# Optimization experiments

Hardware: AMD Instinct MI355X
Metric: run time of the kernel (lower is better)

Reference implementation:

```python
import jax, jax.numpy as jnp
import numpy as np

B, S, E, H = 2, 2048, 1024, 16
DH = E // H


def setup_inputs() -> dict:
    key = jax.random.key(0)
    ks = jax.random.split(key, 7)
    sc = 1.0 / np.sqrt(E)
    return {
        "x": jax.random.normal(ks[0], (B, S, E), dtype=jnp.float32),
        "Wq": jax.random.uniform(ks[1], (E, E), jnp.float32, -sc, sc),
        "bq": jax.random.uniform(ks[2], (E,), jnp.float32, -sc, sc),
        "Wk": jax.random.uniform(ks[3], (E, E), jnp.float32, -sc, sc),
        "bk": jax.random.uniform(ks[4], (E,), jnp.float32, -sc, sc),
        "Wv": jax.random.uniform(ks[5], (E, E), jnp.float32, -sc, sc),
        "bv": jax.random.uniform(ks[6], (E,), jnp.float32, -sc, sc),
    }


def reference(x, Wq, bq, Wk, bk, Wv, bv):
    b, s, _ = x.shape
    # torch Linear: y = x @ W.T + b
    q = (x @ Wq.T + bq).reshape(b, s, H, DH).transpose(0, 2, 1, 3)  # [B,H,S,Dh]
    k = (x @ Wk.T + bk).reshape(b, s, H, DH).transpose(0, 2, 1, 3)
    v = (x @ Wv.T + bv).reshape(b, s, H, DH).transpose(0, 2, 1, 3)
    # original einsum labels treat axis1 as 's' and axis2 as 'h'/'v':
    # scores: [B, S_q, H, S_k]  (softmax over keys, last axis)
    scores = jnp.einsum('bshd,bsvd->bhsv', q, k) / np.sqrt(DH)
    probs = jax.nn.softmax(scores, axis=-1)
    # out: [B, H, S, Dh] per original label permutation
    out = jnp.einsum('bhsv,bsvd->bshd', probs, v)
    # original reshapes WITHOUT transposing heads back (faithful quirk)
    return out.reshape(b, s, E)
```

## Files before the change

### kernel.cpp

```cpp
#include <hip/hip_runtime.h>
#include <hip/hip_bf16.h>

#define Bb 2
#define Ss 2048
#define Ee 1024
#define Hh 16
#define Dh 64
#define QSCALE 0.18033688011112042f

using u16 = unsigned short;
typedef __attribute__((ext_vector_type(8))) short short8;
typedef __attribute__((ext_vector_type(8))) u16 ushort8;
typedef __attribute__((ext_vector_type(4))) float f32x4;

#define GAS __attribute__((address_space(1)))
#define LAS __attribute__((address_space(3)))

__device__ __forceinline__ void gload16(const u16* g, u16* l) {
  __builtin_amdgcn_global_load_lds((const GAS unsigned int*)g,
                                   (LAS unsigned int*)l, 16, 0, 0);
}

__device__ __forceinline__ u16 f2bf(float f) {
  union { float f; unsigned u; } v;
  v.f = f;
  unsigned u = v.u;
  unsigned r = (u + 0x7FFFu + ((u >> 16) & 1u)) >> 16;
  return (u16)r;
}

__global__ __launch_bounds__(256) void cvt_all(
    const float* __restrict__ x, const float* __restrict__ wq,
    const float* __restrict__ wk, const float* __restrict__ wv,
    u16* __restrict__ xo, u16* __restrict__ wqo, u16* __restrict__ wko,
    u16* __restrict__ wvo) {
  const int b = blockIdx.x;
  const float* s;
  u16* d;
  int i;
  if (b < 2048) {
    s = x; d = xo; i = b * 256 + threadIdx.x;
  } else {
    const int wb = b - 2048;
    const int which = wb >> 9;
    s = which == 0 ? wq : (which == 1 ? wk : wv);
    d = which == 0 ? wqo : (which == 1 ? wko : wvo);
    i = (wb & 511) * 256 + threadIdx.x;
  }
  const float* p = s + (size_t)i * 8;
  ushort8 o;
#pragma unroll
  for (int j = 0; j < 8; ++j) o[j] = f2bf(p[j]);
  *(ushort8*)(d + (size_t)i * 8) = o;
}

__global__ __launch_bounds__(256) void qkv_gemm(
    const u16* __restrict__ Xb, const u16* __restrict__ Wcat,
    const float* __restrict__ bq, const float* __restrict__ bk,
    const float* __restrict__ bv,
    u16* __restrict__ Qo, u16* __restrict__ Ko, u16* __restrict__ Vo) {
  __shared__ u16 Ast[128][64];
  __shared__ u16 Bst[128][64];
  const int tid = threadIdx.x;
  const int lane = tid & 63;
  const int w = tid >> 6;
  const int wm = w >> 1, wn = w & 1;
  const int c = lane & 15, g = lane >> 4;
  const int m0 = blockIdx.y * 128;
  const int n0 = blockIdx.x * 128;
  const bool swapv = n0 >= 2048;

  f32x4 acc[4][4] = {};

  for (int kt = 0; kt < 16; ++kt) {
    const int k0 = kt * 64;
    __syncthreads();
#pragma unroll
    for (int i = 0; i < 4; ++i) {
      const int elem = i * 2048 + tid * 8;
      const int row = elem >> 6, col = elem & 63;
      const int lbase = i * 2048 + w * 512;
      gload16(Xb + (size_t)(m0 + row) * 1024 + k0 + col, &Ast[0][0] + lbase);
      gload16(Wcat + (size_t)(n0 + row) * 1024 + k0 + col, &Bst[0][0] + lbase);
    }
    __syncthreads();

#pragma unroll
    for (int ks = 0; ks < 2; ++ks) {
      short8 af[4], bf[4];
#pragma unroll
      for (int mf = 0; mf < 4; ++mf)
        af[mf] = *(const short8*)&Ast[wm * 64 + mf * 16 + c][ks * 32 + g * 8];
#pragma unroll
      for (int nf = 0; nf < 4; ++nf)
        bf[nf] = *(const short8*)&Bst[wn * 64 + nf * 16 + c][ks * 32 + g * 8];
      if (!swapv) {
#pragma unroll
        for (int mf = 0; mf < 4; ++mf)
#pragma unroll
          for (int nf = 0; nf < 4; ++nf)
            acc[mf][nf] = __builtin_amdgcn_mfma_f32_16x16x32_bf16(
                af[mf], bf[nf], acc[mf][nf], 0, 0, 0);
      } else {
#pragma unroll
        for (int mf = 0; mf < 4; ++mf)
#pragma unroll
          for (int nf = 0; nf < 4; ++nf)
            acc[mf][nf] = __builtin_amdgcn_mfma_f32_16x16x32_bf16(
                bf[nf], af[mf], acc[mf][nf], 0, 0, 0);
      }
    }
  }

  if (!swapv) {
    const int which = n0 >> 10;
    u16* Oo = which == 0 ? Qo : Ko;
    const float* bias = which == 0 ? bq : bk;
    const float scl = which == 0 ? QSCALE : 1.0f;
#pragma unroll
    for (int nf = 0; nf < 4; ++nf) {
      const int n = (n0 & 1023) + wn * 64 + nf * 16 + c;
      const float bval = bias[n];
      const int hh = n >> 6, dd = n & 63;
#pragma unroll
      for (int mf = 0; mf < 4; ++mf) {
#pragma unroll
        for (int r = 0; r < 4; ++r) {
          const int m = m0 + wm * 64 + mf * 16 + g * 4 + r;
          const int bb = m >> 11, ss = m & 2047;
          Oo[(((size_t)bb * Hh + hh) * Ss + ss) * Dh + dd] =
              f2bf((acc[mf][nf][r] + bval) * scl);
        }
      }
    }
  } else {
#pragma unroll
    for (int nf = 0; nf < 4; ++nf) {
#pragma unroll
      for (int r = 0; r < 4; ++r) {
        const int n = (n0 - 2048) + wn * 64 + nf * 16 + g * 4 + r;
        const float bval = bv[n];
        const int hh = n >> 6, dd = n & 63;
#pragma unroll
        for (int mf = 0; mf < 4; ++mf) {
          const int m = m0 + wm * 64 + mf * 16 + c;
          const int bb = m >> 11, ss = m & 2047;
          Vo[(((size_t)bb * Hh + hh) * Dh + dd) * Ss + ss] =
              f2bf(acc[mf][nf][r] + bval);
        }
      }
    }
  }
}

__global__ __launch_bounds__(256) void attn(
    const u16* __restrict__ Q, const u16* __restrict__ K,
    const u16* __restrict__ VT, float* __restrict__ out) {
  __shared__ u16 Kst[64][72];
  __shared__ u16 Vt[64][72];
  __shared__ u16 Pst[4][16][72];
  const int tid = threadIdx.x;
  const int lane = tid & 63;
  const int w = tid >> 6;
  const int c = lane & 15, g = lane >> 4;
  const int bh = blockIdx.y;
  const int q0 = blockIdx.x * 64;
  const u16* Qb = Q + (size_t)bh * Ss * Dh;
  const u16* Kb = K + (size_t)bh * Ss * Dh;
  const u16* VTb = VT + (size_t)bh * Ss * Dh;
  const int srow = tid >> 3, sseg = tid & 7;

  short8 aq[2];
  {
#pragma unroll
    for (int it = 0; it < 2; ++it)
      *(ushort8*)&Kst[it * 32 + srow][sseg * 8] =
          *(const ushort8*)(Qb + (size_t)(q0 + it * 32 + srow) * Dh + sseg * 8);
    __syncthreads();
    aq[0] = *(const short8*)&Kst[w * 16 + c][g * 8];
    aq[1] = *(const short8*)&Kst[w * 16 + c][32 + g * 8];
  }

  short8 ones;
#pragma unroll
  for (int j = 0; j < 8; ++j) ones[j] = (short)0x3F80;

  ushort8 kreg[2], vreg[2];
#pragma unroll
  for (int it = 0; it < 2; ++it) {
    kreg[it] = *(const ushort8*)(Kb + (size_t)(it * 32 + srow) * Dh + sseg * 8);
    vreg[it] = *(const ushort8*)(VTb + (size_t)(it * 32 + srow) * Ss + sseg * 8);
  }

  f32x4 oacc[4] = {};
  f32x4 lacc = {};

  for (int kt = 0; kt < 32; ++kt) {
    __syncthreads();
#pragma unroll
    for (int it = 0; it < 2; ++it) {
      *(ushort8*)&Kst[it * 32 + srow][sseg * 8] = kreg[it];
      *(ushort8*)&Vt[it * 32 + srow][sseg * 8] = vreg[it];
    }
    __syncthreads();
    if (kt < 31) {
      const int k0n = (kt + 1) * 64;
#pragma unroll
      for (int it = 0; it < 2; ++it) {
        kreg[it] = *(const ushort8*)(Kb + (size_t)(k0n + it * 32 + srow) * Dh + sseg * 8);
        vreg[it] = *(const ushort8*)(VTb + (size_t)(it * 32 + srow) * Ss + k0n + sseg * 8);
      }
    }

    f32x4 sc[4] = {};
    __builtin_amdgcn_s_setprio(1);
#pragma unroll
    for (int ks = 0; ks < 2; ++ks) {
#pragma unroll
      for (int nt = 0; nt < 4; ++nt) {
        short8 bk_ = *(const short8*)&Kst[nt * 16 + c][ks * 32 + g * 8];
        sc[nt] = __builtin_amdgcn_mfma_f32_16x16x32_bf16(aq[ks], bk_, sc[nt], 0, 0, 0);
      }
    }
    __builtin_amdgcn_s_setprio(0);

#pragma unroll
    for (int nt = 0; nt < 4; ++nt)
#pragma unroll
      for (int r = 0; r < 4; ++r) {
        float p = __builtin_amdgcn_exp2f(sc[nt][r]);
        Pst[w][g * 4 + r][nt * 16 + c] =
            (u16)(__builtin_bit_cast(unsigned, p) >> 16);
      }
    asm volatile("s_waitcnt lgkmcnt(0)" ::: "memory");
    __builtin_amdgcn_sched_barrier(0);

    __builtin_amdgcn_s_setprio(1);
#pragma unroll
    for (int ks = 0; ks < 2; ++ks) {
      short8 pa = *(const short8*)&Pst[w][c][ks * 32 + g * 8];
      lacc = __builtin_amdgcn_mfma_f32_16x16x32_bf16(pa, ones, lacc, 0, 0, 0);
#pragma unroll
      for (int nt2 = 0; nt2 < 4; ++nt2) {
        short8 bv_ = *(const short8*)&Vt[nt2 * 16 + c][ks * 32 + g * 8];
        oacc[nt2] = __builtin_amdgcn_mfma_f32_16x16x32_bf16(pa, bv_, oacc[nt2], 0, 0, 0);
      }
    }
    __builtin_amdgcn_s_setprio(0);
  }

  const size_t obase = (size_t)bh * Ss * Dh;
#pragma unroll
  for (int r = 0; r < 4; ++r) {
    const float inv = 1.0f / lacc[r];
    const int q = q0 + w * 16 + g * 4 + r;
#pragma unroll
    for (int nt2 = 0; nt2 < 4; ++nt2)
      out[obase + (size_t)q * Dh + nt2 * 16 + c] = oacc[nt2][r] * inv;
  }
}

extern "C" void kernel_launch(void* const* d_in, const int* in_sizes, int n_in,
                              void* d_out, int out_size, void* d_ws, size_t ws_size,
                              hipStream_t stream) {
  const float* x = (const float*)d_in[0];
  const float* Wq = (const float*)d_in[1];
  const float* bq = (const float*)d_in[2];
  const float* Wk = (const float*)d_in[3];
  const float* bk = (const float*)d_in[4];
  const float* Wv = (const float*)d_in[5];
  const float* bv = (const float*)d_in[6];
  float* out = (float*)d_out;

  if (ws_size < (size_t)(38u << 20)) return;
  char* ws = (char*)d_ws;
  u16* Qb = (u16*)(ws + (size_t)(0u << 20));
  u16* Kb = (u16*)(ws + (size_t)(8u << 20));
  u16* Vb = (u16*)(ws + (size_t)(16u << 20));
  u16* Xb = (u16*)(ws + (size_t)(24u << 20));
  u16* Wqb = (u16*)(ws + (size_t)(32u << 20));
  u16* Wkb = (u16*)(ws + (size_t)(34u << 20));
  u16* Wvb = (u16*)(ws + (size_t)(36u << 20));

  cvt_all<<<3584, 256, 0, stream>>>(x, Wq, Wk, Wv, Xb, Wqb, Wkb, Wvb);
  qkv_gemm<<<dim3(24, 32), 256, 0, stream>>>(Xb, Wqb, bq, bk, bv, Qb, Kb, Vb);
  attn<<<dim3(32, 32), 256, 0, stream>>>(Qb, Kb, Vb, out);
}
```

Before: 120.5 us.

## Load K/V fragments directly from global and double query rows per block

```diff
diff --git a/kernel.cpp b/kernel.cpp
--- a/kernel.cpp
+++ b/kernel.cpp
@@ -153,97 +153,102 @@
   }
 }
 
-__global__ __launch_bounds__(256) void attn(
+__global__ __launch_bounds__(256, 2) void attn(
     const u16* __restrict__ Q, const u16* __restrict__ K,
     const u16* __restrict__ VT, float* __restrict__ out) {
-  __shared__ u16 Kst[64][72];
-  __shared__ u16 Vt[64][72];
-  __shared__ u16 Pst[4][16][72];
+  __shared__ u16 Pst[4][2][16][72];
   const int tid = threadIdx.x;
   const int lane = tid & 63;
   const int w = tid >> 6;
   const int c = lane & 15, g = lane >> 4;
   const int bh = blockIdx.y;
-  const int q0 = blockIdx.x * 64;
+  const int q0 = blockIdx.x * 128;
   const u16* Qb = Q + (size_t)bh * Ss * Dh;
   const u16* Kb = K + (size_t)bh * Ss * Dh;
   const u16* VTb = VT + (size_t)bh * Ss * Dh;
-  const int srow = tid >> 3, sseg = tid & 7;
-
-  short8 aq[2];
-  {
-#pragma unroll
-    for (int it = 0; it < 2; ++it)
-      *(ushort8*)&Kst[it * 32 + srow][sseg * 8] =
-          *(const ushort8*)(Qb + (size_t)(q0 + it * 32 + srow) * Dh + sseg * 8);
-    __syncthreads();
-    aq[0] = *(const short8*)&Kst[w * 16 + c][g * 8];
-    aq[1] = *(const short8*)&Kst[w * 16 + c][32 + g * 8];
-  }
+
+  short8 aq[2][2];
+#pragma unroll
+  for (int h = 0; h < 2; ++h)
+#pragma unroll
+    for (int ks = 0; ks < 2; ++ks)
+      aq[h][ks] = *(const short8*)(Qb + (size_t)(q0 + h * 64 + w * 16 + c) * Dh +
+                                   ks * 32 + g * 8);
 
   short8 ones;
 #pragma unroll
   for (int j = 0; j < 8; ++j) ones[j] = (short)0x3F80;
 
-  ushort8 kreg[2], vreg[2];
-#pragma unroll
-  for (int it = 0; it < 2; ++it) {
-    kreg[it] = *(const ushort8*)(Kb + (size_t)(it * 32 + srow) * Dh + sseg * 8);
-    vreg[it] = *(const ushort8*)(VTb + (size_t)(it * 32 + srow) * Ss + sseg * 8);
-  }
-
-  f32x4 oacc[4] = {};
-  f32x4 lacc = {};
+  short8 kf[2][4];
+#pragma unroll
+  for (int ks = 0; ks < 2; ++ks)
+#pragma unroll
+    for (int nt = 0; nt < 4; ++nt)
+      kf[ks][nt] = *(const short8*)(Kb + (size_t)(nt * 16 + c) * Dh +
+                                    ks * 32 + g * 8);
+
+  f32x4 oacc[2][4] = {};
+  f32x4 lacc[2] = {};
 
   for (int kt = 0; kt < 32; ++kt) {
-    __syncthreads();
-#pragma unroll
-    for (int it = 0; it < 2; ++it) {
-      *(ushort8*)&Kst[it * 32 + srow][sseg * 8] = kreg[it];
-      *(ushort8*)&Vt[it * 32 + srow][sseg * 8] = vreg[it];
-    }
-    __syncthreads();
+    const int k0 = kt * 64;
+
+    short8 vf[2][4];
+#pragma unroll
+    for (int ks = 0; ks < 2; ++ks)
+#pragma unroll
+      for (int nt = 0; nt < 4; ++nt)
+        vf[ks][nt] = *(const short8*)(VTb + (size_t)(nt * 16 + c) * Ss + k0 +
+                                      ks * 32 + g * 8);
+
+    f32x4 sc[2][4] = {};
+    __builtin_amdgcn_s_setprio(1);
+#pragma unroll
+    for (int ks = 0; ks < 2; ++ks)
+#pragma unroll
+      for (int nt = 0; nt < 4; ++nt) {
+        sc[0][nt] = __builtin_amdgcn_mfma_f32_16x16x32_bf16(aq[0][ks], kf[ks][nt],
+                                                            sc[0][nt], 0, 0, 0);
+        sc[1][nt] = __builtin_amdgcn_mfma_f32_16x16x32_bf16(aq[1][ks], kf[ks][nt],
+                                                            sc[1][nt], 0, 0, 0);
+      }
+    __builtin_amdgcn_s_setprio(0);
+
     if (kt < 31) {
-      const int k0n = (kt + 1) * 64;
-#pragma unroll
-      for (int it = 0; it < 2; ++it) {
-        kreg[it] = *(const ushort8*)(Kb + (size_t)(k0n + it * 32 + srow) * Dh + sseg * 8);
-        vreg[it] = *(const ushort8*)(VTb + (size_t)(it * 32 + srow) * Ss + k0n + sseg * 8);
-      }
-    }
-
-    f32x4 sc[4] = {};
-    __builtin_amdgcn_s_setprio(1);
-#pragma unroll
-    for (int ks = 0; ks < 2; ++ks) {
-#pragma unroll
-      for (int nt = 0; nt < 4; ++nt) {
-        short8 bk_ = *(const short8*)&Kst[nt * 16 + c][ks * 32 + g * 8];
-        sc[nt] = __builtin_amdgcn_mfma_f32_16x16x32_bf16(aq[ks], bk_, sc[nt], 0, 0, 0);
-      }
-    }
-    __builtin_amdgcn_s_setprio(0);
-
-#pragma unroll
-    for (int nt = 0; nt < 4; ++nt)
-#pragma unroll
-      for (int r = 0; r < 4; ++r) {
-        float p = __builtin_amdgcn_exp2f(sc[nt][r]);
-        Pst[w][g * 4 + r][nt * 16 + c] =
-            (u16)(__builtin_bit_cast(unsigned, p) >> 16);
-      }
+#pragma unroll
+      for (int ks = 0; ks < 2; ++ks)
+#pragma unroll
+        for (int nt = 0; nt < 4; ++nt)
+          kf[ks][nt] = *(const short8*)(Kb + (size_t)(k0 + 64 + nt * 16 + c) * Dh +
+                                        ks * 32 + g * 8);
+    }
+
+#pragma unroll
+    for (int h = 0; h < 2; ++h)
+#pragma unroll
+      for (int nt = 0; nt < 4; ++nt)
+#pragma unroll
+        for (int r = 0; r < 4; ++r) {
+          float p = __builtin_amdgcn_exp2f(sc[h][nt][r]);
+          Pst[w][h][g * 4 + r][nt * 16 + c] =
+              (u16)(__builtin_bit_cast(unsigned, p) >> 16);
+        }
     asm volatile("s_waitcnt lgkmcnt(0)" ::: "memory");
     __builtin_amdgcn_sched_barrier(0);
 
     __builtin_amdgcn_s_setprio(1);
 #pragma unroll
     for (int ks = 0; ks < 2; ++ks) {
-      short8 pa = *(const short8*)&Pst[w][c][ks * 32 + g * 8];
-      lacc = __builtin_amdgcn_mfma_f32_16x16x32_bf16(pa, ones, lacc, 0, 0, 0);
+      short8 pa0 = *(const short8*)&Pst[w][0][c][ks * 32 + g * 8];
+      short8 pa1 = *(const short8*)&Pst[w][1][c][ks * 32 + g * 8];
+      lacc[0] = __builtin_amdgcn_mfma_f32_16x16x32_bf16(pa0, ones, lacc[0], 0, 0, 0);
+      lacc[1] = __builtin_amdgcn_mfma_f32_16x16x32_bf16(pa1, ones, lacc[1], 0, 0, 0);
 #pragma unroll
       for (int nt2 = 0; nt2 < 4; ++nt2) {
-        short8 bv_ = *(const short8*)&Vt[nt2 * 16 + c][ks * 32 + g * 8];
-        oacc[nt2] = __builtin_amdgcn_mfma_f32_16x16x32_bf16(pa, bv_, oacc[nt2], 0, 0, 0);
+        oacc[0][nt2] = __builtin_amdgcn_mfma_f32_16x16x32_bf16(pa0, vf[ks][nt2],
+                                                               oacc[0][nt2], 0, 0, 0);
+        oacc[1][nt2] = __builtin_amdgcn_mfma_f32_16x16x32_bf16(pa1, vf[ks][nt2],
+                                                               oacc[1][nt2], 0, 0, 0);
       }
     }
     __builtin_amdgcn_s_setprio(0);
@@ -251,12 +256,15 @@
 
   const size_t obase = (size_t)bh * Ss * Dh;
 #pragma unroll
-  for (int r = 0; r < 4; ++r) {
-    const float inv = 1.0f / lacc[r];
-    const int q = q0 + w * 16 + g * 4 + r;
-#pragma unroll
-    for (int nt2 = 0; nt2 < 4; ++nt2)
-      out[obase + (size_t)q * Dh + nt2 * 16 + c] = oacc[nt2][r] * inv;
+  for (int h = 0; h < 2; ++h) {
+#pragma unroll
+    for (int r = 0; r < 4; ++r) {
+      const float inv = 1.0f / lacc[h][r];
+      const int q = q0 + h * 64 + w * 16 + g * 4 + r;
+#pragma unroll
+      for (int nt2 = 0; nt2 < 4; ++nt2)
+        out[obase + (size_t)q * Dh + nt2 * 16 + c] = oacc[h][nt2][r] * inv;
+    }
   }
 }
 
@@ -284,5 +292,5 @@
 
   cvt_all<<<3584, 256, 0, stream>>>(x, Wq, Wk, Wv, Xb, Wqb, Wkb, Wvb);
   qkv_gemm<<<dim3(24, 32), 256, 0, stream>>>(Xb, Wqb, bq, bk, bv, Qb, Kb, Vb);
-  attn<<<dim3(32, 32), 256, 0, stream>>>(Qb, Kb, Vb, out);
-}
+  attn<<<dim3(16, 32), 256, 0, stream>>>(Qb, Kb, Vb, out);
+}
```

New measurement: 172.9 us. 1.43x slower.

## Rewrite attention with 32x32 MFMA, register-resident P, and double-buffered async K/V loads

Applied to the files above, without the earlier changes.

```diff
diff --git a/kernel.cpp b/kernel.cpp
--- a/kernel.cpp
+++ b/kernel.cpp
@@ -9,9 +9,12 @@
 #define QSCALE 0.18033688011112042f
 
 using u16 = unsigned short;
+using u32 = unsigned int;
 typedef __attribute__((ext_vector_type(8))) short short8;
 typedef __attribute__((ext_vector_type(8))) u16 ushort8;
 typedef __attribute__((ext_vector_type(4))) float f32x4;
+typedef __attribute__((ext_vector_type(16))) float f32x16;
+typedef __attribute__((ext_vector_type(4))) u32 uint4v;
 
 #define GAS __attribute__((address_space(1)))
 #define LAS __attribute__((address_space(3)))
@@ -156,107 +159,128 @@
 __global__ __launch_bounds__(256) void attn(
     const u16* __restrict__ Q, const u16* __restrict__ K,
     const u16* __restrict__ VT, float* __restrict__ out) {
-  __shared__ u16 Kst[64][72];
-  __shared__ u16 Vt[64][72];
-  __shared__ u16 Pst[4][16][72];
+  __shared__ u16 Kst[2][64][64];
+  __shared__ u16 Vst[2][64][64];
+  __shared__ float l_lds[4][32];
   const int tid = threadIdx.x;
   const int lane = tid & 63;
   const int w = tid >> 6;
-  const int c = lane & 15, g = lane >> 4;
+  const int c5 = lane & 31, g2 = lane >> 5;
   const int bh = blockIdx.y;
-  const int q0 = blockIdx.x * 64;
+  const int q0 = blockIdx.x * 128;
   const u16* Qb = Q + (size_t)bh * Ss * Dh;
   const u16* Kb = K + (size_t)bh * Ss * Dh;
   const u16* VTb = VT + (size_t)bh * Ss * Dh;
-  const int srow = tid >> 3, sseg = tid & 7;
-
-  short8 aq[2];
-  {
-#pragma unroll
-    for (int it = 0; it < 2; ++it)
-      *(ushort8*)&Kst[it * 32 + srow][sseg * 8] =
-          *(const ushort8*)(Qb + (size_t)(q0 + it * 32 + srow) * Dh + sseg * 8);
-    __syncthreads();
-    aq[0] = *(const short8*)&Kst[w * 16 + c][g * 8];
-    aq[1] = *(const short8*)&Kst[w * 16 + c][32 + g * 8];
-  }
-
-  short8 ones;
-#pragma unroll
-  for (int j = 0; j < 8; ++j) ones[j] = (short)0x3F80;
-
-  ushort8 kreg[2], vreg[2];
-#pragma unroll
-  for (int it = 0; it < 2; ++it) {
-    kreg[it] = *(const ushort8*)(Kb + (size_t)(it * 32 + srow) * Dh + sseg * 8);
-    vreg[it] = *(const ushort8*)(VTb + (size_t)(it * 32 + srow) * Ss + sseg * 8);
-  }
-
-  f32x4 oacc[4] = {};
-  f32x4 lacc = {};
+
+  const int srow = lane >> 3;
+  const int scolx = ((lane & 7) * 8) ^ (srow * 8);
+
+  const u16* Qrow = Qb + (size_t)(q0 + w * 32 + c5) * Dh + 8 * g2;
+  short8 qf[4];
+#pragma unroll
+  for (int s = 0; s < 4; ++s) qf[s] = *(const short8*)(Qrow + 16 * s);
+
+#pragma unroll
+  for (int p = 0; p < 2; ++p) {
+    const int row = w * 8 + srow + p * 32;
+    gload16(Kb + (size_t)row * Dh + scolx, &Kst[0][0][0] + w * 512 + p * 2048);
+    gload16(VTb + (size_t)row * Ss + scolx, &Vst[0][0][0] + w * 512 + p * 2048);
+  }
+
+  f32x16 oacc0 = {}, oacc1 = {};
+  float lsum = 0.f;
 
   for (int kt = 0; kt < 32; ++kt) {
-    __syncthreads();
-#pragma unroll
-    for (int it = 0; it < 2; ++it) {
-      *(ushort8*)&Kst[it * 32 + srow][sseg * 8] = kreg[it];
-      *(ushort8*)&Vt[it * 32 + srow][sseg * 8] = vreg[it];
-    }
     __syncthreads();
     if (kt < 31) {
       const int k0n = (kt + 1) * 64;
-#pragma unroll
-      for (int it = 0; it < 2; ++it) {
-        kreg[it] = *(const ushort8*)(Kb + (size_t)(k0n + it * 32 + srow) * Dh + sseg * 8);
-        vreg[it] = *(const ushort8*)(VTb + (size_t)(it * 32 + srow) * Ss + k0n + sseg * 8);
+      const int nb = (kt + 1) & 1;
+#pragma unroll
+      for (int p = 0; p < 2; ++p) {
+        const int row = w * 8 + srow + p * 32;
+        gload16(Kb + (size_t)(k0n + row) * Dh + scolx,
+                &Kst[nb][0][0] + w * 512 + p * 2048);
+        gload16(VTb + (size_t)row * Ss + k0n + scolx,
+                &Vst[nb][0][0] + w * 512 + p * 2048);
       }
     }
-
-    f32x4 sc[4] = {};
+    const char* kbuf = (const char*)&Kst[kt & 1][0][0];
+    const char* vbuf = (const char*)&Vst[kt & 1][0][0];
+    const int cxor = (c5 & 7) << 4;
+
+    f32x16 sc0 = {}, sc1 = {};
     __builtin_amdgcn_s_setprio(1);
 #pragma unroll
-    for (int ks = 0; ks < 2; ++ks) {
-#pragma unroll
-      for (int nt = 0; nt < 4; ++nt) {
-        short8 bk_ = *(const short8*)&Kst[nt * 16 + c][ks * 32 + g * 8];
-        sc[nt] = __builtin_amdgcn_mfma_f32_16x16x32_bf16(aq[ks], bk_, sc[nt], 0, 0, 0);
-      }
+    for (int s = 0; s < 4; ++s) {
+      const int cb = (32 * s + 16 * g2) ^ cxor;
+      short8 kf0 = *(const short8*)(kbuf + c5 * 128 + cb);
+      short8 kf1 = *(const short8*)(kbuf + (32 + c5) * 128 + cb);
+      sc0 = __builtin_amdgcn_mfma_f32_32x32x16_bf16(kf0, qf[s], sc0, 0, 0, 0);
+      sc1 = __builtin_amdgcn_mfma_f32_32x32x16_bf16(kf1, qf[s], sc1, 0, 0, 0);
     }
     __builtin_amdgcn_s_setprio(0);
 
-#pragma unroll
-    for (int nt = 0; nt < 4; ++nt)
-#pragma unroll
-      for (int r = 0; r < 4; ++r) {
-        float p = __builtin_amdgcn_exp2f(sc[nt][r]);
-        Pst[w][g * 4 + r][nt * 16 + c] =
-            (u16)(__builtin_bit_cast(unsigned, p) >> 16);
-      }
-    asm volatile("s_waitcnt lgkmcnt(0)" ::: "memory");
-    __builtin_amdgcn_sched_barrier(0);
+    u32 pkv[2][8];
+    float part = 0.f;
+#pragma unroll
+    for (int i = 0; i < 8; ++i) {
+      const u32 e0 = __builtin_bit_cast(u32, __builtin_amdgcn_exp2f(sc0[2 * i]));
+      const u32 e1 = __builtin_bit_cast(u32, __builtin_amdgcn_exp2f(sc0[2 * i + 1]));
+      pkv[0][i] = (e0 >> 16) | (e1 & 0xFFFF0000u);
+      part += __builtin_bit_cast(float, e0 & 0xFFFF0000u) +
+              __builtin_bit_cast(float, e1 & 0xFFFF0000u);
+    }
+#pragma unroll
+    for (int i = 0; i < 8; ++i) {
+      const u32 e0 = __builtin_bit_cast(u32, __builtin_amdgcn_exp2f(sc1[2 * i]));
+      const u32 e1 = __builtin_bit_cast(u32, __builtin_amdgcn_exp2f(sc1[2 * i + 1]));
+      pkv[1][i] = (e0 >> 16) | (e1 & 0xFFFF0000u);
+      part += __builtin_bit_cast(float, e0 & 0xFFFF0000u) +
+              __builtin_bit_cast(float, e1 & 0xFFFF0000u);
+    }
+    lsum += part;
 
     __builtin_amdgcn_s_setprio(1);
 #pragma unroll
-    for (int ks = 0; ks < 2; ++ks) {
-      short8 pa = *(const short8*)&Pst[w][c][ks * 32 + g * 8];
-      lacc = __builtin_amdgcn_mfma_f32_16x16x32_bf16(pa, ones, lacc, 0, 0, 0);
-#pragma unroll
-      for (int nt2 = 0; nt2 < 4; ++nt2) {
-        short8 bv_ = *(const short8*)&Vt[nt2 * 16 + c][ks * 32 + g * 8];
-        oacc[nt2] = __builtin_amdgcn_mfma_f32_16x16x32_bf16(pa, bv_, oacc[nt2], 0, 0, 0);
-      }
+    for (int sp = 0; sp < 4; ++sp) {
+      const int kb = sp >> 1, sg = sp & 1;
+      const u32 a0 = pkv[kb][4 * sg + 0], a1 = pkv[kb][4 * sg + 1];
+      const u32 b0 = pkv[kb][4 * sg + 2], b1 = pkv[kb][4 * sg + 3];
+      const u32 keep0 = g2 ? b0 : a0, keep1 = g2 ? b1 : a1;
+      const u32 send0 = g2 ? a0 : b0, send1 = g2 ? a1 : b1;
+      const u32 recv0 = (u32)__shfl_xor((int)send0, 32);
+      const u32 recv1 = (u32)__shfl_xor((int)send1, 32);
+      uint4v av;
+      av[0] = g2 ? recv0 : keep0;
+      av[1] = g2 ? recv1 : keep1;
+      av[2] = g2 ? keep0 : recv0;
+      av[3] = g2 ? keep1 : recv1;
+      const short8 af = __builtin_bit_cast(short8, av);
+      const int cb = (32 * sp + 16 * g2) ^ cxor;
+      short8 vf0 = *(const short8*)(vbuf + c5 * 128 + cb);
+      short8 vf1 = *(const short8*)(vbuf + (32 + c5) * 128 + cb);
+      oacc0 = __builtin_amdgcn_mfma_f32_32x32x16_bf16(af, vf0, oacc0, 0, 0, 0);
+      oacc1 = __builtin_amdgcn_mfma_f32_32x32x16_bf16(af, vf1, oacc1, 0, 0, 0);
     }
     __builtin_amdgcn_s_setprio(0);
   }
 
-  const size_t obase = (size_t)bh * Ss * Dh;
-#pragma unroll
-  for (int r = 0; r < 4; ++r) {
-    const float inv = 1.0f / lacc[r];
-    const int q = q0 + w * 16 + g * 4 + r;
-#pragma unroll
-    for (int nt2 = 0; nt2 < 4; ++nt2)
-      out[obase + (size_t)q * Dh + nt2 * 16 + c] = oacc[nt2][r] * inv;
+  float ltot = lsum + __shfl_xor(lsum, 32);
+  if (g2 == 0) l_lds[w][c5] = ltot;
+  asm volatile("s_waitcnt lgkmcnt(0)" ::: "memory");
+  __builtin_amdgcn_sched_barrier(0);
+  f32x4 lv[4];
+#pragma unroll
+  for (int t = 0; t < 4; ++t)
+    lv[t] = *(const f32x4*)&l_lds[w][8 * t + 4 * g2];
+
+  float* ob = out + (size_t)bh * Ss * Dh;
+#pragma unroll
+  for (int r = 0; r < 16; ++r) {
+    const float inv = 1.0f / lv[r >> 2][r & 3];
+    const int q = q0 + w * 32 + (r & 3) + 8 * (r >> 2) + 4 * g2;
+    ob[(size_t)q * Dh + c5] = oacc0[r] * inv;
+    ob[(size_t)q * Dh + 32 + c5] = oacc1[r] * inv;
   }
 }
 
@@ -284,5 +308,5 @@
 
   cvt_all<<<3584, 256, 0, stream>>>(x, Wq, Wk, Wv, Xb, Wqb, Wkb, Wvb);
   qkv_gemm<<<dim3(24, 32), 256, 0, stream>>>(Xb, Wqb, bq, bk, bv, Qb, Kb, Vb);
-  attn<<<dim3(32, 32), 256, 0, stream>>>(Qb, Kb, Vb, out);
-}
+  attn<<<dim3(16, 32), 256, 0, stream>>>(Qb, Kb, Vb, out);
+}
```

Result: faster. 113.0 us (-6.2%).
